# Optimization experiments

Hardware: AMD Instinct MI355X
Metric: run time of the kernel (lower is better)

The kernel has to match this reference:

```python
import jax, jax.numpy as jnp
import numpy as np

N_NODES = 50000
N_EDGES = 800000  # random edges, guaranteed no self loops; self loops appended explicitly
D_FEAT = 128
N_LAYERS = 4


def setup_inputs() -> dict:
    key = jax.random.key(0)
    k1, k2, k3, k4 = jax.random.split(key, 4)
    src = jax.random.randint(k1, (N_EDGES,), 0, N_NODES)
    # offset in [1, N-1] guarantees dst != src (module removes self loops anyway)
    off = jax.random.randint(k2, (N_EDGES,), 1, N_NODES)
    dst = (src + off) % N_NODES
    # add_self_loop: append i->i for every node (module does this every layer;
    # with drop_edge p=0 the per-layer graph is identical, so build once)
    loops = jnp.arange(N_NODES)
    src = jnp.concatenate([src, loops])
    dst = jnp.concatenate([dst, loops])
    in_feat = jax.random.normal(k3, (N_NODES, D_FEAT), jnp.float32)
    Ws = jax.random.normal(k4, (N_LAYERS, D_FEAT, D_FEAT), jnp.float32) / np.sqrt(D_FEAT)
    bs = jnp.zeros((N_LAYERS, D_FEAT), jnp.float32)
    return {"in_feat": in_feat, "Ws": Ws, "bs": bs, "src": src, "dst": dst}


def reference(in_feat, Ws, bs, src, dst):
    # JKNet: L x [dropout(p=0) -> GraphConv(norm='both') -> LeakyReLU], then JK max.
    N = in_feat.shape[0]
    ones = jnp.ones(src.shape[0], in_feat.dtype)
    deg_out = jax.ops.segment_sum(ones, src, num_segments=N)  # out-degree (src norm)
    deg_in = jax.ops.segment_sum(ones, dst, num_segments=N)   # in-degree  (dst norm)
    norm_src = jnp.maximum(deg_out, 1.0) ** -0.5
    norm_dst = jnp.maximum(deg_in, 1.0) ** -0.5

    feat_list = [in_feat]
    x = in_feat
    for l in range(Ws.shape[0]):
        h = x * norm_src[:, None]
        agg = jax.ops.segment_sum(h[src], dst, num_segments=N)  # [N, d] sparse aggregation
        h = agg * norm_dst[:, None]
        h = h @ Ws[l] + bs[l]
        x = jax.nn.leaky_relu(h, negative_slope=0.01)  # nn.LeakyReLU default
        feat_list.append(x)

    # Jumping-knowledge max pooling over layer outputs (torch.max values)
    return jnp.max(jnp.stack(feat_list, axis=-1), axis=-1)
```

## Files before the change

kernel.cpp:

```cpp
#include <hip/hip_runtime.h>
#include <cstdint>

#define D 128
#define MAXDEG 64

typedef __attribute__((ext_vector_type(8))) short bf16x8;
typedef __attribute__((ext_vector_type(4))) float f32x4;

__device__ __forceinline__ unsigned short f2b(float f) {
  unsigned u = __float_as_uint(f);
  return (unsigned short)((u + 0x7fffu + ((u >> 16) & 1u)) >> 16);
}
__device__ __forceinline__ float blo(unsigned u) { return __uint_as_float(u << 16); }
__device__ __forceinline__ float bhi(unsigned u) { return __uint_as_float(u & 0xffff0000u); }

__global__ __launch_bounds__(256) void init_kernel(int* __restrict__ cursor,
    int* __restrict__ dego, int N) {
  int i = blockIdx.x * 256 + threadIdx.x;
  if (i < N) {
    cursor[i] = i * MAXDEG;
    dego[i] = 0;
  }
}

__global__ __launch_bounds__(256) void fill_deg(const int* __restrict__ src,
    const int* __restrict__ dst, int* __restrict__ cursor,
    int* __restrict__ esrc, int* __restrict__ dego, int Er) {
  int e = blockIdx.x * 256 + threadIdx.x;
  if (e < Er) {
    int s = src[e];
    int d = dst[e];
    int slot = atomicAdd(cursor + d, 1);
    esrc[slot] = s;
    atomicAdd(dego + s, 1);
  }
}

__global__ __launch_bounds__(256) void norm_kernel(const int* __restrict__ dego,
    const int* __restrict__ cursor, float* __restrict__ ns,
    float* __restrict__ nd, int N) {
  int i = blockIdx.x * 256 + threadIdx.x;
  if (i < N) {
    ns[i] = rsqrtf((float)(dego[i] + 1));
    nd[i] = rsqrtf((float)(cursor[i] - i * MAXDEG + 1));
  }
}

__global__ __launch_bounds__(256) void prep_w(const float* __restrict__ Ws,
    unsigned short* __restrict__ Wt, int total) {
  int i = blockIdx.x * 256 + threadIdx.x;
  if (i < total) {
    int l = i >> 14;
    int rem = i & 16383;
    int k = rem >> 7;
    int c = rem & 127;
    Wt[(l << 14) + (((c << 7) + k) ^ ((c & 7) << 3))] = f2b(Ws[i]);
  }
}

template<bool INF32>
__global__ __launch_bounds__(256, 4) void gemm_mfma(const float* __restrict__ xf,
    const unsigned short* __restrict__ xb, const float* __restrict__ nsrc,
    const unsigned short* __restrict__ Wt, unsigned short* __restrict__ zout,
    int N) {
  __shared__ unsigned short Wl[D * D];
  {
    const uint4* s4 = (const uint4*)Wt;
    uint4* d4 = (uint4*)Wl;
    #pragma unroll
    for (int i = 0; i < 8; ++i) d4[threadIdx.x + i * 256] = s4[threadIdx.x + i * 256];
  }
  __syncthreads();

  int wave = threadIdx.x >> 6;
  int lane = threadIdx.x & 63;
  int r16 = lane & 15;
  int kgrp = lane >> 4;
  int rw0 = blockIdx.x * 128 + wave * 16;
  int rw1 = rw0 + 64;

  f32x4 acc0[8] = {};
  f32x4 acc1[8] = {};
  int gr0 = rw0 + r16; if (gr0 >= N) gr0 = N - 1;
  int gr1 = rw1 + r16; if (gr1 >= N) gr1 = N - 1;

  #pragma unroll
  for (int ks = 0; ks < 4; ++ks) {
    int k0 = ks * 32 + kgrp * 8;
    bf16x8 a0, a1;
    if (INF32) {
      const float4* p0 = (const float4*)(xf + (size_t)gr0 * D + k0);
      float4 lo = p0[0], hi = p0[1];
      a0[0] = (short)f2b(lo.x); a0[1] = (short)f2b(lo.y);
      a0[2] = (short)f2b(lo.z); a0[3] = (short)f2b(lo.w);
      a0[4] = (short)f2b(hi.x); a0[5] = (short)f2b(hi.y);
      a0[6] = (short)f2b(hi.z); a0[7] = (short)f2b(hi.w);
      const float4* p1 = (const float4*)(xf + (size_t)gr1 * D + k0);
      lo = p1[0]; hi = p1[1];
      a1[0] = (short)f2b(lo.x); a1[1] = (short)f2b(lo.y);
      a1[2] = (short)f2b(lo.z); a1[3] = (short)f2b(lo.w);
      a1[4] = (short)f2b(hi.x); a1[5] = (short)f2b(hi.y);
      a1[6] = (short)f2b(hi.z); a1[7] = (short)f2b(hi.w);
    } else {
      a0 = *(const bf16x8*)(xb + (size_t)gr0 * D + k0);
      a1 = *(const bf16x8*)(xb + (size_t)gr1 * D + k0);
    }
    #pragma unroll
    for (int ct = 0; ct < 8; ++ct) {
      int c = ct * 16 + r16;
      bf16x8 b = *(const bf16x8*)(Wl + (((c << 7) + k0) ^ ((c & 7) << 3)));
      acc0[ct] = __builtin_amdgcn_mfma_f32_16x16x32_bf16(a0, b, acc0[ct], 0, 0, 0);
      acc1[ct] = __builtin_amdgcn_mfma_f32_16x16x32_bf16(a1, b, acc1[ct], 0, 0, 0);
    }
  }

  #pragma unroll
  for (int q = 0; q < 4; ++q) {
    int row0 = rw0 + kgrp * 4 + q;
    if (row0 < N) {
      float ns = nsrc[row0];
      #pragma unroll
      for (int ct = 0; ct < 8; ++ct)
        zout[(size_t)row0 * D + ct * 16 + r16] = f2b(acc0[ct][q] * ns);
    }
    int row1 = rw1 + kgrp * 4 + q;
    if (row1 < N) {
      float ns = nsrc[row1];
      #pragma unroll
      for (int ct = 0; ct < 8; ++ct)
        zout[(size_t)row1 * D + ct * 16 + r16] = f2b(acc1[ct][q] * ns);
    }
  }
}

struct Acc8 {
  float a0, a1, a2, a3, a4, a5, a6, a7;
  __device__ __forceinline__ void zero() {
    a0 = a1 = a2 = a3 = a4 = a5 = a6 = a7 = 0.f;
  }
  __device__ __forceinline__ void add(uint4 v) {
    a0 += blo(v.x); a1 += bhi(v.x); a2 += blo(v.y); a3 += bhi(v.y);
    a4 += blo(v.z); a5 += bhi(v.z); a6 += blo(v.w); a7 += bhi(v.w);
  }
};

template<bool INJ32, bool OUTJ32>
__global__ __launch_bounds__(256, 8) void gather_kernel(
    const unsigned short* __restrict__ z, const int* __restrict__ row_end,
    const int* __restrict__ esrc, const float* __restrict__ ndst,
    const float* __restrict__ bias, const float* __restrict__ jkinf,
    const unsigned short* __restrict__ jkinb, unsigned short* __restrict__ xb_out,
    float* __restrict__ jkoutf, unsigned short* __restrict__ jkoutb,
    int N, int write_x) {
  int t = blockIdx.x * 256 + threadIdx.x;
  int row = t >> 4;
  if (row >= N) return;
  int cg = t & 15;
  const uint4* zp = (const uint4*)z;

  int b = row * MAXDEG;
  int e = row_end[row];
  Acc8 A;
  A.zero();
  A.add(zp[(size_t)row * 16 + cg]);

  int j = b;
  for (; j + 3 < e; j += 4) {
    int4 s = *(const int4*)(esrc + j);
    uint4 v0 = zp[(size_t)s.x * 16 + cg];
    uint4 v1 = zp[(size_t)s.y * 16 + cg];
    uint4 v2 = zp[(size_t)s.z * 16 + cg];
    uint4 v3 = zp[(size_t)s.w * 16 + cg];
    A.add(v0); A.add(v1); A.add(v2); A.add(v3);
  }
  for (; j < e; ++j) {
    A.add(zp[(size_t)esrc[j] * 16 + cg]);
  }

  float nd = ndst[row];
  float4 bv0 = ((const float4*)bias)[cg * 2];
  float4 bv1 = ((const float4*)bias)[cg * 2 + 1];
  float4 o0, o1;
  o0.x = nd * A.a0 + bv0.x; o0.y = nd * A.a1 + bv0.y;
  o0.z = nd * A.a2 + bv0.z; o0.w = nd * A.a3 + bv0.w;
  o1.x = nd * A.a4 + bv1.x; o1.y = nd * A.a5 + bv1.y;
  o1.z = nd * A.a6 + bv1.z; o1.w = nd * A.a7 + bv1.w;
  o0.x = o0.x > 0.f ? o0.x : 0.01f * o0.x;
  o0.y = o0.y > 0.f ? o0.y : 0.01f * o0.y;
  o0.z = o0.z > 0.f ? o0.z : 0.01f * o0.z;
  o0.w = o0.w > 0.f ? o0.w : 0.01f * o0.w;
  o1.x = o1.x > 0.f ? o1.x : 0.01f * o1.x;
  o1.y = o1.y > 0.f ? o1.y : 0.01f * o1.y;
  o1.z = o1.z > 0.f ? o1.z : 0.01f * o1.z;
  o1.w = o1.w > 0.f ? o1.w : 0.01f * o1.w;

  if (write_x) {
    uint4 px;
    px.x = (unsigned)f2b(o0.x) | ((unsigned)f2b(o0.y) << 16);
    px.y = (unsigned)f2b(o0.z) | ((unsigned)f2b(o0.w) << 16);
    px.z = (unsigned)f2b(o1.x) | ((unsigned)f2b(o1.y) << 16);
    px.w = (unsigned)f2b(o1.z) | ((unsigned)f2b(o1.w) << 16);
    ((uint4*)xb_out)[(size_t)row * 16 + cg] = px;
  }

  float4 m0, m1;
  if (INJ32) {
    m0 = ((const float4*)jkinf)[(size_t)row * 32 + cg * 2];
    m1 = ((const float4*)jkinf)[(size_t)row * 32 + cg * 2 + 1];
  } else {
    uint4 mj = ((const uint4*)jkinb)[(size_t)row * 16 + cg];
    m0.x = blo(mj.x); m0.y = bhi(mj.x); m0.z = blo(mj.y); m0.w = bhi(mj.y);
    m1.x = blo(mj.z); m1.y = bhi(mj.z); m1.z = blo(mj.w); m1.w = bhi(mj.w);
  }
  m0.x = fmaxf(m0.x, o0.x); m0.y = fmaxf(m0.y, o0.y);
  m0.z = fmaxf(m0.z, o0.z); m0.w = fmaxf(m0.w, o0.w);
  m1.x = fmaxf(m1.x, o1.x); m1.y = fmaxf(m1.y, o1.y);
  m1.z = fmaxf(m1.z, o1.z); m1.w = fmaxf(m1.w, o1.w);
  if (OUTJ32) {
    ((float4*)jkoutf)[(size_t)row * 32 + cg * 2] = m0;
    ((float4*)jkoutf)[(size_t)row * 32 + cg * 2 + 1] = m1;
  } else {
    uint4 pm;
    pm.x = (unsigned)f2b(m0.x) | ((unsigned)f2b(m0.y) << 16);
    pm.y = (unsigned)f2b(m0.z) | ((unsigned)f2b(m0.w) << 16);
    pm.z = (unsigned)f2b(m1.x) | ((unsigned)f2b(m1.y) << 16);
    pm.w = (unsigned)f2b(m1.z) | ((unsigned)f2b(m1.w) << 16);
    ((uint4*)jkoutb)[(size_t)row * 16 + cg] = pm;
  }
}

extern "C" void kernel_launch(void* const* d_in, const int* in_sizes, int n_in,
                              void* d_out, int out_size, void* d_ws, size_t ws_size,
                              hipStream_t stream) {
  const float* in_feat = (const float*)d_in[0];
  const float* Ws = (const float*)d_in[1];
  const float* bs = (const float*)d_in[2];
  const int* src = (const int*)d_in[3];
  const int* dst = (const int*)d_in[4];
  int N = in_sizes[0] / D;
  int L = in_sizes[2] / D;
  int E = in_sizes[3];
  float* out = (float*)d_out;

  int Er = E - N;
  if (Er < 0) Er = E;

  int nb = (N + 255) / 256;

  char* p = (char*)d_ws;
  int* dego   = (int*)p;   p += (size_t)N * 4;
  int* cursor = (int*)p;   p += (size_t)N * 4;
  int* esrc   = (int*)p;   p += (size_t)N * MAXDEG * 4;
  float* nsrc = (float*)p; p += (size_t)N * 4;
  float* ndst = (float*)p; p += (size_t)N * 4;
  unsigned short* wt  = (unsigned short*)p; p += (size_t)L * D * D * 2;
  unsigned short* z   = (unsigned short*)p; p += (size_t)N * D * 2;
  unsigned short* xb  = (unsigned short*)p; p += (size_t)N * D * 2;
  unsigned short* jkb = (unsigned short*)p;

  init_kernel<<<nb, 256, 0, stream>>>(cursor, dego, N);
  fill_deg<<<(Er + 255) / 256, 256, 0, stream>>>(src, dst, cursor, esrc, dego, Er);
  norm_kernel<<<nb, 256, 0, stream>>>(dego, cursor, nsrc, ndst, N);
  int wtot = L * D * D;
  prep_w<<<(wtot + 255) / 256, 256, 0, stream>>>(Ws, wt, wtot);

  int mb = (N + 127) / 128;
  int gb = (int)(((long long)N * 16 + 255) / 256);
  for (int l = 0; l < L; ++l) {
    const unsigned short* wl = wt + (size_t)l * D * D;
    if (l == 0) {
      gemm_mfma<true><<<mb, 256, 0, stream>>>(in_feat, nullptr, nsrc, wl, z, N);
    } else {
      gemm_mfma<false><<<mb, 256, 0, stream>>>(nullptr, xb, nsrc, wl, z, N);
    }
    const float* bias = bs + (size_t)l * D;
    int wx = (l + 1 < L) ? 1 : 0;
    if (l == 0 && L == 1) {
      gather_kernel<true, true><<<gb, 256, 0, stream>>>(z, cursor, esrc,
          ndst, bias, in_feat, nullptr, xb, out, nullptr, N, wx);
    } else if (l == 0) {
      gather_kernel<true, false><<<gb, 256, 0, stream>>>(z, cursor, esrc,
          ndst, bias, in_feat, nullptr, xb, nullptr, jkb, N, wx);
    } else if (l == L - 1) {
      gather_kernel<false, true><<<gb, 256, 0, stream>>>(z, cursor, esrc,
          ndst, bias, nullptr, jkb, xb, out, nullptr, N, wx);
    } else {
      gather_kernel<false, false><<<gb, 256, 0, stream>>>(z, cursor, esrc,
          ndst, bias, nullptr, jkb, xb, nullptr, jkb, N, wx);
    }
  }
}
```

Before: 276.0 us.

## Split gather into four column-slab passes over a slab-major Z layout

The GEMM now writes Z in four column slabs of 32 features each (slab-major), and the gather runs as four passes, one per slab, with 4 threads per row instead of 16. Each pass touches a 3.2 MB slab of Z, which fits in the L2/LLC, so the random neighbor gathers should hit cache more often. The cost is re-reading the edge lists and norms four times and launching four times as many kernels, each with less memory-level parallelism per row.

Measured after the change: 356.6 us. +29.2%, slower.

```diff
diff --git a/kernel.cpp b/kernel.cpp
--- a/kernel.cpp
+++ b/kernel.cpp
@@ -121,14 +121,16 @@
       float ns = nsrc[row0];
       #pragma unroll
       for (int ct = 0; ct < 8; ++ct)
-        zout[(size_t)row0 * D + ct * 16 + r16] = f2b(acc0[ct][q] * ns);
+        zout[(size_t)(ct >> 1) * N * 32 + (size_t)row0 * 32 + (ct & 1) * 16 + r16]
+            = f2b(acc0[ct][q] * ns);
     }
     int row1 = rw1 + kgrp * 4 + q;
     if (row1 < N) {
       float ns = nsrc[row1];
       #pragma unroll
       for (int ct = 0; ct < 8; ++ct)
-        zout[(size_t)row1 * D + ct * 16 + r16] = f2b(acc1[ct][q] * ns);
+        zout[(size_t)(ct >> 1) * N * 32 + (size_t)row1 * 32 + (ct & 1) * 16 + r16]
+            = f2b(acc1[ct][q] * ns);
     }
   }
 }
@@ -145,41 +147,42 @@
 };
 
 template<bool INJ32, bool OUTJ32>
-__global__ __launch_bounds__(256, 8) void gather_kernel(
-    const unsigned short* __restrict__ z, const int* __restrict__ row_end,
-    const int* __restrict__ esrc, const float* __restrict__ ndst,
-    const float* __restrict__ bias, const float* __restrict__ jkinf,
-    const unsigned short* __restrict__ jkinb, unsigned short* __restrict__ xb_out,
-    float* __restrict__ jkoutf, unsigned short* __restrict__ jkoutb,
-    int N, int write_x) {
+__global__ __launch_bounds__(256, 8) void gather_pass(
+    const unsigned short* __restrict__ zb,
+    const int* __restrict__ row_end, const int* __restrict__ esrc,
+    const float* __restrict__ ndst, const float* __restrict__ bias,
+    const float* __restrict__ jkinf, const unsigned short* __restrict__ jkinb,
+    unsigned short* __restrict__ xb_out, float* __restrict__ jkoutf,
+    unsigned short* __restrict__ jkoutb, int N, int write_x, int p) {
   int t = blockIdx.x * 256 + threadIdx.x;
-  int row = t >> 4;
+  int row = t >> 2;
   if (row >= N) return;
-  int cg = t & 15;
-  const uint4* zp = (const uint4*)z;
+  int lq = t & 3;
+  const uint4* zp = (const uint4*)zb;
 
   int b = row * MAXDEG;
   int e = row_end[row];
   Acc8 A;
   A.zero();
-  A.add(zp[(size_t)row * 16 + cg]);
+  A.add(zp[(size_t)row * 4 + lq]);
 
   int j = b;
   for (; j + 3 < e; j += 4) {
     int4 s = *(const int4*)(esrc + j);
-    uint4 v0 = zp[(size_t)s.x * 16 + cg];
-    uint4 v1 = zp[(size_t)s.y * 16 + cg];
-    uint4 v2 = zp[(size_t)s.z * 16 + cg];
-    uint4 v3 = zp[(size_t)s.w * 16 + cg];
+    uint4 v0 = zp[(size_t)s.x * 4 + lq];
+    uint4 v1 = zp[(size_t)s.y * 4 + lq];
+    uint4 v2 = zp[(size_t)s.z * 4 + lq];
+    uint4 v3 = zp[(size_t)s.w * 4 + lq];
     A.add(v0); A.add(v1); A.add(v2); A.add(v3);
   }
   for (; j < e; ++j) {
-    A.add(zp[(size_t)esrc[j] * 16 + cg]);
+    A.add(zp[(size_t)esrc[j] * 4 + lq]);
   }
 
   float nd = ndst[row];
-  float4 bv0 = ((const float4*)bias)[cg * 2];
-  float4 bv1 = ((const float4*)bias)[cg * 2 + 1];
+  int cb = p * 8 + lq * 2;
+  float4 bv0 = ((const float4*)bias)[cb];
+  float4 bv1 = ((const float4*)bias)[cb + 1];
   float4 o0, o1;
   o0.x = nd * A.a0 + bv0.x; o0.y = nd * A.a1 + bv0.y;
   o0.z = nd * A.a2 + bv0.z; o0.w = nd * A.a3 + bv0.w;
@@ -200,15 +203,15 @@
     px.y = (unsigned)f2b(o0.z) | ((unsigned)f2b(o0.w) << 16);
     px.z = (unsigned)f2b(o1.x) | ((unsigned)f2b(o1.y) << 16);
     px.w = (unsigned)f2b(o1.z) | ((unsigned)f2b(o1.w) << 16);
-    ((uint4*)xb_out)[(size_t)row * 16 + cg] = px;
+    ((uint4*)xb_out)[(size_t)row * 16 + p * 4 + lq] = px;
   }
 
   float4 m0, m1;
   if (INJ32) {
-    m0 = ((const float4*)jkinf)[(size_t)row * 32 + cg * 2];
-    m1 = ((const float4*)jkinf)[(size_t)row * 32 + cg * 2 + 1];
+    m0 = ((const float4*)jkinf)[(size_t)row * 32 + cb];
+    m1 = ((const float4*)jkinf)[(size_t)row * 32 + cb + 1];
   } else {
-    uint4 mj = ((const uint4*)jkinb)[(size_t)row * 16 + cg];
+    uint4 mj = ((const uint4*)jkinb)[(size_t)row * 16 + p * 4 + lq];
     m0.x = blo(mj.x); m0.y = bhi(mj.x); m0.z = blo(mj.y); m0.w = bhi(mj.y);
     m1.x = blo(mj.z); m1.y = bhi(mj.z); m1.z = blo(mj.w); m1.w = bhi(mj.w);
   }
@@ -217,15 +220,15 @@
   m1.x = fmaxf(m1.x, o1.x); m1.y = fmaxf(m1.y, o1.y);
   m1.z = fmaxf(m1.z, o1.z); m1.w = fmaxf(m1.w, o1.w);
   if (OUTJ32) {
-    ((float4*)jkoutf)[(size_t)row * 32 + cg * 2] = m0;
-    ((float4*)jkoutf)[(size_t)row * 32 + cg * 2 + 1] = m1;
+    ((float4*)jkoutf)[(size_t)row * 32 + cb] = m0;
+    ((float4*)jkoutf)[(size_t)row * 32 + cb + 1] = m1;
   } else {
     uint4 pm;
     pm.x = (unsigned)f2b(m0.x) | ((unsigned)f2b(m0.y) << 16);
     pm.y = (unsigned)f2b(m0.z) | ((unsigned)f2b(m0.w) << 16);
     pm.z = (unsigned)f2b(m1.x) | ((unsigned)f2b(m1.y) << 16);
     pm.w = (unsigned)f2b(m1.z) | ((unsigned)f2b(m1.w) << 16);
-    ((uint4*)jkoutb)[(size_t)row * 16 + cg] = pm;
+    ((uint4*)jkoutb)[(size_t)row * 16 + p * 4 + lq] = pm;
   }
 }
 
@@ -265,7 +268,7 @@
   prep_w<<<(wtot + 255) / 256, 256, 0, stream>>>(Ws, wt, wtot);
 
   int mb = (N + 127) / 128;
-  int gb = (int)(((long long)N * 16 + 255) / 256);
+  int gb = (int)(((long long)N * 4 + 255) / 256);
   for (int l = 0; l < L; ++l) {
     const unsigned short* wl = wt + (size_t)l * D * D;
     if (l == 0) {
@@ -275,18 +278,21 @@
     }
     const float* bias = bs + (size_t)l * D;
     int wx = (l + 1 < L) ? 1 : 0;
-    if (l == 0 && L == 1) {
-      gather_kernel<true, true><<<gb, 256, 0, stream>>>(z, cursor, esrc,
-          ndst, bias, in_feat, nullptr, xb, out, nullptr, N, wx);
-    } else if (l == 0) {
-      gather_kernel<true, false><<<gb, 256, 0, stream>>>(z, cursor, esrc,
-          ndst, bias, in_feat, nullptr, xb, nullptr, jkb, N, wx);
-    } else if (l == L - 1) {
-      gather_kernel<false, true><<<gb, 256, 0, stream>>>(z, cursor, esrc,
-          ndst, bias, nullptr, jkb, xb, out, nullptr, N, wx);
-    } else {
-      gather_kernel<false, false><<<gb, 256, 0, stream>>>(z, cursor, esrc,
-          ndst, bias, nullptr, jkb, xb, nullptr, jkb, N, wx);
-    }
-  }
-}
+    for (int ps = 0; ps < 4; ++ps) {
+      const unsigned short* zb = z + (size_t)ps * N * 32;
+      if (l == 0 && L == 1) {
+        gather_pass<true, true><<<gb, 256, 0, stream>>>(zb, cursor, esrc,
+            ndst, bias, in_feat, nullptr, xb, out, nullptr, N, wx, ps);
+      } else if (l == 0) {
+        gather_pass<true, false><<<gb, 256, 0, stream>>>(zb, cursor, esrc,
+            ndst, bias, in_feat, nullptr, xb, nullptr, jkb, N, wx, ps);
+      } else if (l == L - 1) {
+        gather_pass<false, true><<<gb, 256, 0, stream>>>(zb, cursor, esrc,
+            ndst, bias, nullptr, jkb, xb, out, nullptr, N, wx, ps);
+      } else {
+        gather_pass<false, false><<<gb, 256, 0, stream>>>(zb, cursor, esrc,
+            ndst, bias, nullptr, jkb, xb, nullptr, jkb, N, wx, ps);
+      }
+    }
+  }
+}
```
